# Performance work log

Measured on AMD Instinct MI355X. Metric: run time of the kernel, lower is better.

## Reference

```python
import jax, jax.numpy as jnp
import numpy as np
import math

HIDDEN = 2048
HEADS = 16
HEAD_DIM = HIDDEN // HEADS
SEQ = 2048
BATCH = 1
THRESH = 0.7


def setup_inputs() -> dict:
    key = jax.random.key(0)
    ks = jax.random.split(key, 9)
    init = lambda k, shape: (jax.random.normal(k, shape, dtype=jnp.float32) * 0.02)
    return {
        "hidden_states": jax.random.normal(ks[0], (BATCH, SEQ, HIDDEN), dtype=jnp.float32),
        "Wq": init(ks[1], (HIDDEN, HIDDEN)), "bq": jnp.zeros((HIDDEN,), jnp.float32),
        "Wk": init(ks[2], (HIDDEN, HIDDEN)), "bk": jnp.zeros((HIDDEN,), jnp.float32),
        "Wv": init(ks[3], (HIDDEN, HIDDEN)), "bv": jnp.zeros((HIDDEN,), jnp.float32),
        "Wo": init(ks[4], (HIDDEN, HIDDEN)), "bo": jnp.zeros((HIDDEN,), jnp.float32),
        "truth_gate": jnp.full((1,), THRESH, jnp.float32),
        "balance_gate": jnp.full((1,), THRESH, jnp.float32),
        "order_gate": jnp.full((1,), THRESH, jnp.float32),
        "justice_gate": jnp.full((1,), THRESH, jnp.float32),
        "harmony_gate": jnp.full((1,), THRESH, jnp.float32),
    }


def reference(hidden_states, Wq, bq, Wk, bk, Wv, bv, Wo, bo,
              truth_gate, balance_gate, order_gate, justice_gate, harmony_gate):
    B, S, D = hidden_states.shape
    H, hd = HEADS, HEAD_DIM
    # projections -> [B, H, S, hd]
    def proj(W, b):
        return (hidden_states @ W.T + b).reshape(B, S, H, hd).transpose(0, 2, 1, 3)
    q, k, v = proj(Wq, bq), proj(Wk, bk), proj(Wv, bv)

    scores = jnp.einsum('bhqd,bhkd->bhqk', q, k) / math.sqrt(hd)  # [B,H,S,S]

    # truth: penalize by key norm, broadcast over query axis? No -- k_norm is [B,H,S,1],
    # matching torch broadcasting: per-QUERY-row constant (k indexed like q rows).
    truth_penalty = jax.nn.sigmoid(truth_gate) * (jnp.linalg.norm(k, axis=-1, keepdims=True) * 0.01)

    # balance: row entropy of softmax(scores)
    logp = jax.nn.log_softmax(scores, axis=-1)
    entropy = -jnp.sum(jnp.exp(logp) * logp, axis=-1, keepdims=True)  # [B,H,S,1]
    balance_adjustment = jax.nn.sigmoid(balance_gate) * (entropy / math.log(S) * 0.1)

    # order: position bias over the LAST (key) axis, shape [1,1,S] in torch -> broadcasts on key dim
    position_bias = jnp.arange(S, dtype=jnp.float32) / S  # [S]
    order_bonus = jax.nn.sigmoid(order_gate) * (position_bias * 0.05)  # broadcasts over bhq,k

    # justice: pull scores toward their row mean
    mean_score = scores.mean(axis=-1, keepdims=True)
    justice_adjustment = jax.nn.sigmoid(justice_gate) * ((mean_score - scores) * 0.1)

    # harmony: negative mean abs diff along key axis, per row
    smoothness = -jnp.abs(scores[..., 1:] - scores[..., :-1]).mean(axis=-1, keepdims=True)
    harmony_smooth = jax.nn.sigmoid(harmony_gate) * (smoothness * 0.1)

    scores = scores - truth_penalty + balance_adjustment + order_bonus + justice_adjustment + harmony_smooth

    attn = jax.nn.softmax(scores, axis=-1)
    out = jnp.einsum('bhqk,bhkd->bhqd', attn, v)  # [B,H,S,hd]
    out = out.transpose(0, 2, 1, 3).reshape(B, S, D)
    return out @ Wo.T + bo
```

## Files before the change

kernel.cpp:

```cpp
#include <hip/hip_runtime.h>

typedef __bf16 bf16x8 __attribute__((ext_vector_type(8)));
typedef __bf16 bf16x4 __attribute__((ext_vector_type(4)));
typedef float f32x4 __attribute__((ext_vector_type(4)));

typedef const __attribute__((address_space(1))) void* gas_t;
typedef __attribute__((address_space(3))) void* las_t;

static constexpr int DIM = 2048;
static constexpr size_t MAT = (size_t)DIM * DIM;

__device__ __forceinline__ float sigmoidf_(float x) { return 1.f / (1.f + __expf(-x)); }

__global__ void cvt_kernel(const float* __restrict__ x, const float* __restrict__ wq,
                           const float* __restrict__ wk, const float* __restrict__ wv,
                           const float* __restrict__ wo, __bf16* __restrict__ dst) {
  const float* s;
  switch (blockIdx.y) {
    case 0: s = x; break;
    case 1: s = wq; break;
    case 2: s = wk; break;
    case 3: s = wv; break;
    default: s = wo; break;
  }
  __bf16* d = dst + (size_t)blockIdx.y * MAT;
  size_t i = ((size_t)blockIdx.x * 256 + threadIdx.x) * 4;
  float4 v = *(const float4*)(s + i);
  bf16x4 ov;
  ov[0] = (__bf16)v.x; ov[1] = (__bf16)v.y; ov[2] = (__bf16)v.z; ov[3] = (__bf16)v.w;
  *(bf16x4*)(d + i) = ov;
}

template <bool F32OUT>
__device__ __forceinline__ void gemm128(const __bf16* __restrict__ A, const __bf16* __restrict__ B,
                                        const float* __restrict__ bias, bool bias_row, float scale,
                                        void* __restrict__ Cout, int mtile, int ntile,
                                        __bf16* Asm, __bf16* Bsm) {
  const int t = threadIdx.x, lane = t & 63, w = t >> 6;
  const int wrow = (w >> 1) * 64, wcol = (w & 1) * 64;
  const int rbase = mtile * 128, cbase = ntile * 128;
  f32x4 acc[4][4] = {};

  for (int k0 = 0; k0 < DIM; k0 += 32) {
    __syncthreads();
#pragma unroll
    for (int i = 0; i < 2; ++i) {
      const int o = i * 4096 + w * 1024 + lane * 16;
      const int r = o >> 6;
      const int ke = (o & 63) >> 1;
      __builtin_amdgcn_global_load_lds((gas_t)(A + (size_t)(rbase + r) * DIM + k0 + ke),
                                       (las_t)(Asm + (o >> 1)), 16, 0, 0);
      __builtin_amdgcn_global_load_lds((gas_t)(B + (size_t)(cbase + r) * DIM + k0 + ke),
                                       (las_t)(Bsm + (o >> 1)), 16, 0, 0);
    }
    __syncthreads();

    bf16x8 af[4], bf[4];
#pragma unroll
    for (int i = 0; i < 4; ++i)
      af[i] = *(const bf16x8*)(Asm + (wrow + i * 16 + (lane & 15)) * 32 + (lane >> 4) * 8);
#pragma unroll
    for (int j = 0; j < 4; ++j)
      bf[j] = *(const bf16x8*)(Bsm + (wcol + j * 16 + (lane & 15)) * 32 + (lane >> 4) * 8);
#pragma unroll
    for (int i = 0; i < 4; ++i)
#pragma unroll
      for (int j = 0; j < 4; ++j)
        acc[i][j] = __builtin_amdgcn_mfma_f32_16x16x32_bf16(af[i], bf[j], acc[i][j], 0, 0, 0);
  }

#pragma unroll
  for (int i = 0; i < 4; ++i)
#pragma unroll
    for (int j = 0; j < 4; ++j)
#pragma unroll
      for (int r = 0; r < 4; ++r) {
        const int row = rbase + wrow + i * 16 + (lane >> 4) * 4 + r;
        const int col = cbase + wcol + j * 16 + (lane & 15);
        float v = acc[i][j][r] + (bias_row ? bias[row] : bias[col]);
        v *= scale;
        if (F32OUT)
          ((float*)Cout)[(size_t)row * DIM + col] = v;
        else
          ((__bf16*)Cout)[(size_t)row * DIM + col] = (__bf16)v;
      }
}

__global__ __launch_bounds__(256, 2) void qkv_kernel(
    const __bf16* __restrict__ Xb, const __bf16* __restrict__ Wqb, const __bf16* __restrict__ Wkb,
    const __bf16* __restrict__ Wvb, const float* __restrict__ bq, const float* __restrict__ bk,
    const float* __restrict__ bv, const float* __restrict__ jgate, __bf16* __restrict__ Qo,
    __bf16* __restrict__ Ko, __bf16* __restrict__ Vto) {
  __shared__ __bf16 Asm[128 * 32];
  __shared__ __bf16 Bsm[128 * 32];
  const int sel = blockIdx.x >> 4, nt = blockIdx.x & 15, mt = blockIdx.y;
  const __bf16 *A, *B;
  const float* bias;
  __bf16* C;
  bool brow = false;
  float sc = 1.f;
  if (sel == 0) {
    A = Xb; B = Wqb; bias = bq; C = Qo;
    sc = (1.f - 0.1f * sigmoidf_(jgate[0])) * 0.08838834764831843f;
  } else if (sel == 1) {
    A = Xb; B = Wkb; bias = bk; C = Ko;
  } else {
    A = Wvb; B = Xb; bias = bv; C = Vto; brow = true;
  }
  gemm128<false>(A, B, bias, brow, sc, C, mt, nt, Asm, Bsm);
}

__global__ __launch_bounds__(256, 2) void outproj_kernel(const __bf16* __restrict__ Ab,
                                                         const __bf16* __restrict__ Wob,
                                                         const float* __restrict__ bo,
                                                         float* __restrict__ Cout) {
  __shared__ __bf16 Asm[128 * 32];
  __shared__ __bf16 Bsm[128 * 32];
  gemm128<true>(Ab, Wob, bo, false, 1.f, Cout, blockIdx.y, blockIdx.x, Asm, Bsm);
}

__global__ __launch_bounds__(512) void attn_kernel(const __bf16* __restrict__ Q,
                                                   const __bf16* __restrict__ Kg,
                                                   const __bf16* __restrict__ VT,
                                                   const float* __restrict__ ogate,
                                                   __bf16* __restrict__ O) {
  __shared__ __bf16 Ks[4 * 64 * 32];
  __shared__ __bf16 Vs[2 * 128 * 32];
  __shared__ __bf16 Ps[8 * 16 * 72];
  const int t = threadIdx.x, lane = t & 63, w = t >> 6;
  const int h = blockIdx.y, qt = blockIdx.x;
  const float beta = sigmoidf_(ogate[0]) * 0.05f / 2048.0f;

  const int qrow = qt * 128 + w * 16 + (lane & 15);
  bf16x8 qf[4];
#pragma unroll
  for (int c = 0; c < 4; ++c)
    qf[c] = *(const bf16x8*)(Q + (size_t)qrow * DIM + h * 128 + c * 32 + (lane >> 4) * 8);

  f32x4 oacc[8] = {};
  float m_r[4], l_r[4];
#pragma unroll
  for (int r = 0; r < 4; ++r) { m_r[r] = -1e30f; l_r[r] = 0.f; }

  for (int kt = 0; kt < 2048; kt += 64) {
    __syncthreads();
#pragma unroll
    for (int i = 0; i < 2; ++i) {
      const int o = i * 8192 + w * 1024 + lane * 16;
      const int ke = (o & 63) >> 1;
      const int c = o >> 12, key = (o & 4095) >> 6;
      __builtin_amdgcn_global_load_lds((gas_t)(Kg + (size_t)(kt + key) * DIM + h * 128 + c * 32 + ke),
                                       (las_t)(Ks + (o >> 1)), 16, 0, 0);
      const int d = (o & 8191) >> 6;
      __builtin_amdgcn_global_load_lds((gas_t)(VT + (size_t)(h * 128 + d) * DIM + kt + i * 32 + ke),
                                       (las_t)(Vs + (o >> 1)), 16, 0, 0);
    }
    __syncthreads();

    f32x4 s[4];
#pragma unroll
    for (int j = 0; j < 4; ++j) {
      f32x4 a = {};
#pragma unroll
      for (int c = 0; c < 4; ++c) {
        bf16x8 kf = *(const bf16x8*)(Ks + c * 2048 + (j * 16 + (lane & 15)) * 32 + (lane >> 4) * 8);
        a = __builtin_amdgcn_mfma_f32_16x16x32_bf16(qf[c], kf, a, 0, 0, 0);
      }
      s[j] = a;
    }
#pragma unroll
    for (int j = 0; j < 4; ++j) {
      const float pb = beta * (float)(kt + j * 16 + (lane & 15));
#pragma unroll
      for (int r = 0; r < 4; ++r) s[j][r] += pb;
    }
    float rmax[4];
#pragma unroll
    for (int r = 0; r < 4; ++r)
      rmax[r] = fmaxf(fmaxf(s[0][r], s[1][r]), fmaxf(s[2][r], s[3][r]));
#pragma unroll
    for (int msk = 1; msk < 16; msk <<= 1)
#pragma unroll
      for (int r = 0; r < 4; ++r) rmax[r] = fmaxf(rmax[r], __shfl_xor(rmax[r], msk, 64));

    float al[4];
#pragma unroll
    for (int r = 0; r < 4; ++r) {
      const float mn = fmaxf(m_r[r], rmax[r]);
      al[r] = __expf(m_r[r] - mn);
      m_r[r] = mn;
    }
#pragma unroll
    for (int j = 0; j < 4; ++j)
#pragma unroll
      for (int r = 0; r < 4; ++r) s[j][r] = __expf(s[j][r] - m_r[r]);

    float rs[4];
#pragma unroll
    for (int r = 0; r < 4; ++r) rs[r] = (s[0][r] + s[1][r]) + (s[2][r] + s[3][r]);
#pragma unroll
    for (int msk = 1; msk < 16; msk <<= 1)
#pragma unroll
      for (int r = 0; r < 4; ++r) rs[r] += __shfl_xor(rs[r], msk, 64);
#pragma unroll
    for (int r = 0; r < 4; ++r) l_r[r] = l_r[r] * al[r] + rs[r];
#pragma unroll
    for (int d = 0; d < 8; ++d)
#pragma unroll
      for (int r = 0; r < 4; ++r) oacc[d][r] *= al[r];

    {
      __bf16* pw = Ps + w * 1152;
#pragma unroll
      for (int j = 0; j < 4; ++j)
#pragma unroll
        for (int r = 0; r < 4; ++r)
          pw[((lane >> 4) * 4 + r) * 72 + j * 16 + (lane & 15)] = (__bf16)s[j][r];
    }
    __syncthreads();

#pragma unroll
    for (int cc = 0; cc < 2; ++cc) {
      bf16x8 pa = *(const bf16x8*)(Ps + w * 1152 + (lane & 15) * 72 + cc * 32 + (lane >> 4) * 8);
#pragma unroll
      for (int d = 0; d < 8; ++d) {
        bf16x8 vf = *(const bf16x8*)(Vs + cc * 4096 + (d * 16 + (lane & 15)) * 32 + (lane >> 4) * 8);
        oacc[d] = __builtin_amdgcn_mfma_f32_16x16x32_bf16(pa, vf, oacc[d], 0, 0, 0);
      }
    }
  }

#pragma unroll
  for (int d = 0; d < 8; ++d)
#pragma unroll
    for (int r = 0; r < 4; ++r) {
      const int row = qt * 128 + w * 16 + (lane >> 4) * 4 + r;
      const int col = h * 128 + d * 16 + (lane & 15);
      O[(size_t)row * DIM + col] = (__bf16)(oacc[d][r] / l_r[r]);
    }
}

extern "C" void kernel_launch(void* const* d_in, const int* in_sizes, int n_in,
                              void* d_out, int out_size, void* d_ws, size_t ws_size,
                              hipStream_t stream) {
  const float* X  = (const float*)d_in[0];
  const float* Wq = (const float*)d_in[1];
  const float* bq = (const float*)d_in[2];
  const float* Wk = (const float*)d_in[3];
  const float* bk = (const float*)d_in[4];
  const float* Wv = (const float*)d_in[5];
  const float* bv = (const float*)d_in[6];
  const float* Wo = (const float*)d_in[7];
  const float* bo = (const float*)d_in[8];
  const float* order_g   = (const float*)d_in[11];
  const float* justice_g = (const float*)d_in[12];

  __bf16* wsb = (__bf16*)d_ws;
  __bf16* Xb  = wsb + 0 * MAT;
  __bf16* Wqb = wsb + 1 * MAT;
  __bf16* Wkb = wsb + 2 * MAT;
  __bf16* Wvb = wsb + 3 * MAT;
  __bf16* Wob = wsb + 4 * MAT;
  __bf16* Qb  = wsb + 5 * MAT;
  __bf16* Kb  = wsb + 6 * MAT;
  __bf16* VTb = wsb + 7 * MAT;
  __bf16* Ab  = Xb;

  cvt_kernel<<<dim3(4096, 5), 256, 0, stream>>>(X, Wq, Wk, Wv, Wo, wsb);
  qkv_kernel<<<dim3(48, 16), 256, 0, stream>>>(Xb, Wqb, Wkb, Wvb, bq, bk, bv, justice_g,
                                               Qb, Kb, VTb);
  attn_kernel<<<dim3(16, 16), 512, 0, stream>>>(Qb, Kb, VTb, order_g, Ab);
  outproj_kernel<<<dim3(16, 16), 256, 0, stream>>>(Ab, Wob, bo, (float*)d_out);
}
```

Baseline: 333.7 us.

## Double-buffer K/V tiles in attention and swizzle LDS layout

The attention kernel now keeps two LDS buffers for the K and V tiles. It issues the global-to-LDS load of the next key tile right after the loop-top barrier, so that load overlaps the QK^T, softmax and PV work on the current tile. The load addresses are XOR-swizzled so that MFMA fragment reads from LDS cause fewer bank conflicts. The per-iteration barrier count drops from three to one, since the per-warp P scratch needs only wave-local ordering. In exchange, K/V LDS use doubles, which may lower occupancy.

Result: faster. 315.5 us (-5.5%).

```diff
diff --git a/kernel.cpp b/kernel.cpp
--- a/kernel.cpp
+++ b/kernel.cpp
@@ -124,13 +124,15 @@
                                                    const __bf16* __restrict__ VT,
                                                    const float* __restrict__ ogate,
                                                    __bf16* __restrict__ O) {
-  __shared__ __bf16 Ks[4 * 64 * 32];
-  __shared__ __bf16 Vs[2 * 128 * 32];
+  __shared__ __bf16 Ks[2][4 * 64 * 32];
+  __shared__ __bf16 Vs[2][2 * 128 * 32];
   __shared__ __bf16 Ps[8 * 16 * 72];
   const int t = threadIdx.x, lane = t & 63, w = t >> 6;
   const int h = blockIdx.y, qt = blockIdx.x;
   const float beta = sigmoidf_(ogate[0]) * 0.05f / 2048.0f;
 
+  const int rs8 = (((lane >> 4) ^ ((lane >> 1) & 3)) & 3) * 8;
+
   const int qrow = qt * 128 + w * 16 + (lane & 15);
   bf16x8 qf[4];
 #pragma unroll
@@ -142,20 +144,28 @@
 #pragma unroll
   for (int r = 0; r < 4; ++r) { m_r[r] = -1e30f; l_r[r] = 0.f; }
 
+  auto stage = [&](int buf, int kt) {
+#pragma unroll
+    for (int i = 0; i < 2; ++i) {
+      const int o = i * 8192 + w * 1024 + lane * 16;
+      const int oz = o ^ (((o >> 7) & 3) << 4);
+      const int ke = (oz & 63) >> 1;
+      const int c = oz >> 12, key = (oz & 4095) >> 6;
+      __builtin_amdgcn_global_load_lds(
+          (gas_t)(Kg + (size_t)(kt + key) * DIM + h * 128 + c * 32 + ke),
+          (las_t)(&Ks[buf][0] + (o >> 1)), 16, 0, 0);
+      const int cc = oz >> 13, d = (oz & 8191) >> 6;
+      __builtin_amdgcn_global_load_lds(
+          (gas_t)(VT + (size_t)(h * 128 + d) * DIM + kt + cc * 32 + ke),
+          (las_t)(&Vs[buf][0] + (o >> 1)), 16, 0, 0);
+    }
+  };
+
+  stage(0, 0);
+  int p = 0;
   for (int kt = 0; kt < 2048; kt += 64) {
     __syncthreads();
-#pragma unroll
-    for (int i = 0; i < 2; ++i) {
-      const int o = i * 8192 + w * 1024 + lane * 16;
-      const int ke = (o & 63) >> 1;
-      const int c = o >> 12, key = (o & 4095) >> 6;
-      __builtin_amdgcn_global_load_lds((gas_t)(Kg + (size_t)(kt + key) * DIM + h * 128 + c * 32 + ke),
-                                       (las_t)(Ks + (o >> 1)), 16, 0, 0);
-      const int d = (o & 8191) >> 6;
-      __builtin_amdgcn_global_load_lds((gas_t)(VT + (size_t)(h * 128 + d) * DIM + kt + i * 32 + ke),
-                                       (las_t)(Vs + (o >> 1)), 16, 0, 0);
-    }
-    __syncthreads();
+    if (kt + 64 < 2048) stage(p ^ 1, kt + 64);
 
     f32x4 s[4];
 #pragma unroll
@@ -163,7 +173,7 @@
       f32x4 a = {};
 #pragma unroll
       for (int c = 0; c < 4; ++c) {
-        bf16x8 kf = *(const bf16x8*)(Ks + c * 2048 + (j * 16 + (lane & 15)) * 32 + (lane >> 4) * 8);
+        bf16x8 kf = *(const bf16x8*)(&Ks[p][0] + c * 2048 + (j * 16 + (lane & 15)) * 32 + rs8);
         a = __builtin_amdgcn_mfma_f32_16x16x32_bf16(qf[c], kf, a, 0, 0, 0);
       }
       s[j] = a;
@@ -217,17 +227,17 @@
         for (int r = 0; r < 4; ++r)
           pw[((lane >> 4) * 4 + r) * 72 + j * 16 + (lane & 15)] = (__bf16)s[j][r];
     }
-    __syncthreads();
 
 #pragma unroll
     for (int cc = 0; cc < 2; ++cc) {
       bf16x8 pa = *(const bf16x8*)(Ps + w * 1152 + (lane & 15) * 72 + cc * 32 + (lane >> 4) * 8);
 #pragma unroll
       for (int d = 0; d < 8; ++d) {
-        bf16x8 vf = *(const bf16x8*)(Vs + cc * 4096 + (d * 16 + (lane & 15)) * 32 + (lane >> 4) * 8);
+        bf16x8 vf = *(const bf16x8*)(&Vs[p][0] + cc * 4096 + (d * 16 + (lane & 15)) * 32 + rs8);
         oacc[d] = __builtin_amdgcn_mfma_f32_16x16x32_bf16(pa, vf, oacc[d], 0, 0, 0);
       }
     }
+    p ^= 1;
   }
 
 #pragma unroll
```
